# Optimization experiments

Hardware: AMD Instinct MI355X
Metric: run time of the kernel (lower is better)

Reference implementation:

```python
import jax, jax.numpy as jnp
import numpy as np

N = 100000      # nodes
E = 1600000     # edges (avg degree 16)
F_IN = 128      # num_node_features
H = 128         # hidden_size
C = 64          # num_classes


def sage_conv(x, src, dst, W_l, W_r, b, num_nodes):
    """PyG SAGEConv (mean aggr): out = lin_l(mean_{j->i} x_j) + lin_r(x_i) + b."""
    msg = x[src]                                                  # [E, F] gather
    agg = jax.ops.segment_sum(msg, dst, num_segments=num_nodes)   # [N, F] scatter-add
    deg = jax.ops.segment_sum(jnp.ones((src.shape[0],), x.dtype), dst,
                              num_segments=num_nodes)             # [N]
    agg = agg / jnp.maximum(deg, 1.0)[:, None]                    # mean (safe for isolated nodes)
    return agg @ W_l + x @ W_r + b


def setup_inputs() -> dict:
    key = jax.random.key(0)
    ks = jax.random.split(key, 8)
    x = jax.random.normal(ks[0], (N, F_IN), dtype=jnp.float32)
    edge_index = jax.random.randint(ks[1], (2, E), 0, N, dtype=jnp.int32).astype(jnp.int64)
    W1_l = jax.random.normal(ks[2], (F_IN, H), dtype=jnp.float32) / np.float32(np.sqrt(F_IN))
    W1_r = jax.random.normal(ks[3], (F_IN, H), dtype=jnp.float32) / np.float32(np.sqrt(F_IN))
    b1 = jnp.zeros((H,), jnp.float32)
    W2_l = jax.random.normal(ks[4], (H, C), dtype=jnp.float32) / np.float32(np.sqrt(H))
    W2_r = jax.random.normal(ks[5], (H, C), dtype=jnp.float32) / np.float32(np.sqrt(H))
    b2 = jnp.zeros((C,), jnp.float32)
    return {"x": x, "edge_index": edge_index,
            "W1_l": W1_l, "W1_r": W1_r, "b1": b1,
            "W2_l": W2_l, "W2_r": W2_r, "b2": b2}


def reference(x, edge_index, W1_l, W1_r, b1, W2_l, W2_r, b2):
    src, dst = edge_index[0], edge_index[1]
    h = jax.nn.relu(sage_conv(x, src, dst, W1_l, W1_r, b1, N))   # dropout: eval mode => identity
    logits = sage_conv(h, src, dst, W2_l, W2_r, b2, N)
    return jax.nn.log_softmax(logits, axis=1)
```

## Files before the change

### kernel.cpp

```cpp
#include <hip/hip_runtime.h>

#define Nn 100000
#define Ee 1600000
#define FIN 128
#define HID 128
#define CLS 64
#define NB 196
#define BCAP 9216

typedef unsigned short ushort_t;
typedef unsigned int uint_t;
typedef __attribute__((ext_vector_type(8))) short bf16x8;
typedef __attribute__((ext_vector_type(4))) float f32x4;

__device__ __forceinline__ ushort_t f2bf(float f) {
    uint_t u = __float_as_uint(f);
    return (ushort_t)((u + 0x7fffu + ((u >> 16) & 1u)) >> 16);
}
__device__ __forceinline__ float bflo(uint_t u) { return __uint_as_float(u << 16); }
__device__ __forceinline__ float bfhi(uint_t u) { return __uint_as_float(u & 0xffff0000u); }


__global__ __launch_bounds__(1024) void k_front(const int* __restrict__ src,
                                                const int* __restrict__ dst,
                                                int* __restrict__ bcur,
                                                uint2* __restrict__ bedge,
                                                const float* __restrict__ x,
                                                ushort_t* __restrict__ xb,
                                                const float* __restrict__ W1l,
                                                const float* __restrict__ W1r,
                                                const float* __restrict__ W2l,
                                                const float* __restrict__ W2r,
                                                ushort_t* __restrict__ w1lt,
                                                ushort_t* __restrict__ w1rt,
                                                ushort_t* __restrict__ w2lt,
                                                ushort_t* __restrict__ w2rt) {
    __shared__ int h[NB];
    __shared__ int lbase[NB];
    int b = blockIdx.x;
    int t = threadIdx.x;
    if (b < NB) {
        if (t < NB) h[t] = 0;
        __syncthreads();
        int base = b * 8192;
        int bk[8], loc[8];
        #pragma unroll
        for (int it = 0; it < 8; ++it) {
            int e = base + it * 1024 + t;
            if (e < Ee) {
                bk[it] = dst[e] >> 9;
                loc[it] = atomicAdd(&h[bk[it]], 1);
            }
        }
        __syncthreads();
        if (t < NB && h[t]) lbase[t] = atomicAdd(&bcur[t], h[t]);
        __syncthreads();
        #pragma unroll
        for (int it = 0; it < 8; ++it) {
            int e = base + it * 1024 + t;
            if (e < Ee) {
                int pos = lbase[bk[it]] + loc[it];
                if (pos < BCAP)
                    bedge[(size_t)bk[it] * BCAP + pos] = make_uint2((uint_t)src[e], (uint_t)dst[e]);
            }
        }
    } else if (b < NB + 3125) {
        int i = (b - NB) * 1024 + t;
        float4 v = reinterpret_cast<const float4*>(x)[i];
        ushort4 o;
        o.x = f2bf(v.x); o.y = f2bf(v.y); o.z = f2bf(v.z); o.w = f2bf(v.w);
        reinterpret_cast<ushort4*>(xb)[i] = o;
    } else {
        int j = b - (NB + 3125);
        const float* Wsrc; ushort_t* Wdst; int Ncols; int cb;
        if (j < 16)      { Wsrc = W1l; Wdst = w1lt; Ncols = 128; cb = j; }
        else if (j < 32) { Wsrc = W1r; Wdst = w1rt; Ncols = 128; cb = j - 16; }
        else if (j < 40) { Wsrc = W2l; Wdst = w2lt; Ncols = 64;  cb = j - 32; }
        else             { Wsrc = W2r; Wdst = w2rt; Ncols = 64;  cb = j - 40; }
        int i = cb * 1024 + t;
        if (i < 128 * Ncols) {
            int k = i / Ncols, n = i % Ncols;
            Wdst[(size_t)n * 128 + k] = f2bf(Wsrc[i]);
        }
    }
}

__global__ __launch_bounds__(256) void k_bscan(const int* __restrict__ bcur,
                                               int* __restrict__ bstart,
                                               int* __restrict__ rowptr) {
    __shared__ int s[256];
    int t = threadIdx.x;
    int v = (t < NB) ? min(bcur[t], BCAP) : 0;
    s[t] = v;
    __syncthreads();
    for (int off = 1; off < 256; off <<= 1) {
        int u = (t >= off) ? s[t - off] : 0;
        __syncthreads();
        s[t] += u;
        __syncthreads();
    }
    if (t < NB) bstart[t] = s[t] - v;
    if (t == NB - 1) { bstart[NB] = s[t]; rowptr[Nn] = s[t]; }
}

__global__ __launch_bounds__(1024) void k_fillB(const uint2* __restrict__ bedge,
                                                const int* __restrict__ bcur,
                                                const int* __restrict__ bstart,
                                                int* __restrict__ rowptr,
                                                int* __restrict__ csr) {
    __shared__ int h[512];
    __shared__ int off[512];
    int b = blockIdx.x, t = threadIdx.x;
    if (t < 512) h[t] = 0;
    __syncthreads();
    int n = min(bcur[b], BCAP);
    int node0 = b << 9;
    const uint2* be = bedge + (size_t)b * BCAP;
    for (int i = t; i < n; i += 1024)
        atomicAdd(&h[(int)be[i].y - node0], 1);
    __syncthreads();
    if (t < 512) off[t] = h[t];
    __syncthreads();
    for (int o = 1; o < 512; o <<= 1) {
        int v = (t < 512 && t >= o) ? off[t - o] : 0;
        __syncthreads();
        if (t < 512) off[t] += v;
        __syncthreads();
    }
    int base_ = bstart[b];
    if (t < 512) {
        int excl = off[t] - h[t];
        int node = node0 + t;
        if (node < Nn) rowptr[node] = base_ + excl;
        h[t] = excl;
    }
    __syncthreads();
    for (int i = t; i < n; i += 1024) {
        uint2 ed = be[i];
        int loc = atomicAdd(&h[(int)ed.y - node0], 1);
        csr[base_ + loc] = (int)ed.x;
    }
}


__global__ __launch_bounds__(256) void k_agg1(const ushort_t* __restrict__ xb,
                                              const int* __restrict__ rowptr,
                                              const int* __restrict__ csr,
                                              ushort_t* __restrict__ outb) {
    int wid = (blockIdx.x * blockDim.x + threadIdx.x) >> 6;
    int lane = threadIdx.x & 63;
    if (wid >= Nn) return;
    int s0 = __builtin_amdgcn_readfirstlane(rowptr[wid]);
    int s1 = __builtin_amdgcn_readfirstlane(rowptr[wid + 1]);
    float ax = 0.f, ay = 0.f;
    int e = s0;
    for (; e + 16 <= s1; e += 16) {
        int idx[16];
        #pragma unroll
        for (int j = 0; j < 16; ++j) idx[j] = __builtin_amdgcn_readfirstlane(csr[e + j]);
        uint_t u[16];
        #pragma unroll
        for (int j = 0; j < 16; ++j)
            u[j] = *reinterpret_cast<const uint_t*>(xb + (size_t)idx[j] * 128 + lane * 2);
        #pragma unroll
        for (int j = 0; j < 16; ++j) { ax += bflo(u[j]); ay += bfhi(u[j]); }
    }
    for (; e + 8 <= s1; e += 8) {
        int idx[8];
        #pragma unroll
        for (int j = 0; j < 8; ++j) idx[j] = __builtin_amdgcn_readfirstlane(csr[e + j]);
        uint_t u[8];
        #pragma unroll
        for (int j = 0; j < 8; ++j)
            u[j] = *reinterpret_cast<const uint_t*>(xb + (size_t)idx[j] * 128 + lane * 2);
        #pragma unroll
        for (int j = 0; j < 8; ++j) { ax += bflo(u[j]); ay += bfhi(u[j]); }
    }
    for (; e < s1; ++e) {
        int s = __builtin_amdgcn_readfirstlane(csr[e]);
        uint_t u = *reinterpret_cast<const uint_t*>(xb + (size_t)s * 128 + lane * 2);
        ax += bflo(u); ay += bfhi(u);
    }
    float invd = (s1 > s0) ? 1.0f / (float)(s1 - s0) : 0.0f;
    uint_t o = (uint_t)f2bf(ax * invd) | ((uint_t)f2bf(ay * invd) << 16);
    *reinterpret_cast<uint_t*>(outb + (size_t)wid * 128 + lane * 2) = o;
}


__global__ __launch_bounds__(512) void k_gemm1m(const ushort_t* __restrict__ Ab0,
                                                const ushort_t* __restrict__ Ab1,
                                                const ushort_t* __restrict__ Wt0,
                                                const ushort_t* __restrict__ Wt1,
                                                const float* __restrict__ bias,
                                                ushort_t* __restrict__ hb) {
    __shared__ ushort_t lw[2 * 16384];
    const int tid = threadIdx.x;
    char* lwc = reinterpret_cast<char*>(lw);
    #pragma unroll
    for (int i = 0; i < 8; ++i) {
        int c = tid + i * 512;
        int pair = c >> 11;
        int col = (c & 2047) >> 4;
        int kc = c & 15;
        const ushort_t* Wsrc = pair ? Wt1 : Wt0;
        uint4 v = *reinterpret_cast<const uint4*>(Wsrc + col * 128 + kc * 8);
        int dst = ((pair << 15) | (col << 8) | (kc << 4)) ^ ((col & 7) << 4);
        *reinterpret_cast<uint4*>(lwc + dst) = v;
    }
    __syncthreads();

    int gw = (blockIdx.x * 512 + tid) >> 6;
    int lane = tid & 63;
    if (gw >= Nn / 16) return;
    int row0 = gw * 16;
    int r = lane & 15;
    int kg = lane >> 4;
    f32x4 acc[8];
    #pragma unroll
    for (int c = 0; c < 8; ++c) acc[c] = (f32x4){0.f, 0.f, 0.f, 0.f};
    #pragma unroll
    for (int pair = 0; pair < 2; ++pair) {
        const ushort_t* A = pair ? Ab1 : Ab0;
        #pragma unroll
        for (int ks = 0; ks < 4; ++ks) {
            int kbase = ks * 32 + kg * 8;
            bf16x8 af = *reinterpret_cast<const bf16x8*>(A + (size_t)(row0 + r) * 128 + kbase);
            #pragma unroll
            for (int c = 0; c < 8; ++c) {
                int boff = ((pair << 15) | ((c * 16 + r) << 8) | (ks * 64 + kg * 16))
                           ^ ((r & 7) << 4);
                bf16x8 bf = *reinterpret_cast<const bf16x8*>(lwc + boff);
                acc[c] = __builtin_amdgcn_mfma_f32_16x16x32_bf16(af, bf, acc[c], 0, 0, 0);
            }
        }
    }
    #pragma unroll
    for (int c = 0; c < 8; ++c) {
        float bv = bias[c * 16 + r];
        #pragma unroll
        for (int i = 0; i < 4; ++i) {
            int row = row0 + kg * 4 + i;
            hb[(size_t)row * 128 + c * 16 + r] = f2bf(fmaxf(acc[c][i] + bv, 0.f));
        }
    }
}

__global__ __launch_bounds__(256) void k_gemm2f(const ushort_t* __restrict__ Ab,
                                                const ushort_t* __restrict__ Wtl,
                                                const ushort_t* __restrict__ Wtr,
                                                ushort_t* __restrict__ tb,
                                                float* __restrict__ outu) {
    int gw = (blockIdx.x * 256 + threadIdx.x) >> 6;
    int lane = threadIdx.x & 63;
    if (gw >= Nn / 16) return;
    int row0 = gw * 16;
    int r = lane & 15;
    int kg = lane >> 4;
    f32x4 accL[4], accR[4];
    #pragma unroll
    for (int c = 0; c < 4; ++c) {
        accL[c] = (f32x4){0.f, 0.f, 0.f, 0.f};
        accR[c] = (f32x4){0.f, 0.f, 0.f, 0.f};
    }
    #pragma unroll
    for (int ks = 0; ks < 4; ++ks) {
        int kbase = ks * 32 + kg * 8;
        bf16x8 af = *reinterpret_cast<const bf16x8*>(Ab + (size_t)(row0 + r) * 128 + kbase);
        #pragma unroll
        for (int c = 0; c < 4; ++c) {
            bf16x8 bl = *reinterpret_cast<const bf16x8*>(Wtl + (size_t)(c * 16 + r) * 128 + kbase);
            accL[c] = __builtin_amdgcn_mfma_f32_16x16x32_bf16(af, bl, accL[c], 0, 0, 0);
            bf16x8 br = *reinterpret_cast<const bf16x8*>(Wtr + (size_t)(c * 16 + r) * 128 + kbase);
            accR[c] = __builtin_amdgcn_mfma_f32_16x16x32_bf16(af, br, accR[c], 0, 0, 0);
        }
    }
    #pragma unroll
    for (int c = 0; c < 4; ++c) {
        #pragma unroll
        for (int i = 0; i < 4; ++i) {
            int row = row0 + kg * 4 + i;
            tb[(size_t)row * 64 + c * 16 + r] = f2bf(accL[c][i]);
            outu[(size_t)row * 64 + c * 16 + r] = accR[c][i];
        }
    }
}


__global__ __launch_bounds__(256) void k_logsm(float* __restrict__ out,
                                               const ushort_t* __restrict__ tb,
                                               const int* __restrict__ rowptr,
                                               const int* __restrict__ csr,
                                               const float* __restrict__ bias) {
    int wid = (blockIdx.x * blockDim.x + threadIdx.x) >> 6;
    int lane = threadIdx.x & 63;
    if (wid >= Nn) return;
    int s0 = __builtin_amdgcn_readfirstlane(rowptr[wid]);
    int s1 = __builtin_amdgcn_readfirstlane(rowptr[wid + 1]);
    float a = 0.f;
    int e = s0;
    for (; e + 16 <= s1; e += 16) {
        int idx[16];
        #pragma unroll
        for (int j = 0; j < 16; ++j) idx[j] = __builtin_amdgcn_readfirstlane(csr[e + j]);
        ushort_t u[16];
        #pragma unroll
        for (int j = 0; j < 16; ++j) u[j] = tb[(size_t)idx[j] * 64 + lane];
        #pragma unroll
        for (int j = 0; j < 16; ++j) a += __uint_as_float(((uint_t)u[j]) << 16);
    }
    for (; e + 8 <= s1; e += 8) {
        int idx[8];
        #pragma unroll
        for (int j = 0; j < 8; ++j) idx[j] = __builtin_amdgcn_readfirstlane(csr[e + j]);
        ushort_t u[8];
        #pragma unroll
        for (int j = 0; j < 8; ++j) u[j] = tb[(size_t)idx[j] * 64 + lane];
        #pragma unroll
        for (int j = 0; j < 8; ++j) a += __uint_as_float(((uint_t)u[j]) << 16);
    }
    for (; e < s1; ++e) {
        int s = __builtin_amdgcn_readfirstlane(csr[e]);
        a += __uint_as_float(((uint_t)tb[(size_t)s * 64 + lane]) << 16);
    }
    float invd = (s1 > s0) ? 1.0f / (float)(s1 - s0) : 0.0f;
    size_t o = (size_t)wid * 64 + lane;
    float v = (out[o] + a * invd) + bias[lane];
    float m = v;
    #pragma unroll
    for (int off = 32; off; off >>= 1) m = fmaxf(m, __shfl_xor(m, off));
    float ex = __expf(v - m);
    float s_ = ex;
    #pragma unroll
    for (int off = 32; off; off >>= 1) s_ += __shfl_xor(s_, off);
    out[o] = v - m - __logf(s_);
}


extern "C" void kernel_launch(void* const* d_in, const int* in_sizes, int n_in,
                              void* d_out, int out_size, void* d_ws, size_t ws_size,
                              hipStream_t stream) {
    const float* x   = (const float*)d_in[0];
    const int*   ei  = (const int*)d_in[1];
    const float* W1l = (const float*)d_in[2];
    const float* W1r = (const float*)d_in[3];
    const float* b1  = (const float*)d_in[4];
    const float* W2l = (const float*)d_in[5];
    const float* W2r = (const float*)d_in[6];
    const float* b2  = (const float*)d_in[7];
    float* out = (float*)d_out;

    char* ws = (char*)d_ws;
    int*      bstart = (int*)(ws + 0);
    int*      rowptr = (int*)(ws + 800768);
    int*      csr    = (int*)(ws + 1201152);
    ushort_t* xb     = (ushort_t*)(ws + 7601152);
    ushort_t* aggb   = (ushort_t*)(ws + 33201152);
    ushort_t* w1lt   = (ushort_t*)(ws + 58801152);
    ushort_t* w1rt   = (ushort_t*)(ws + 58833920);
    ushort_t* w2lt   = (ushort_t*)(ws + 58866688);
    ushort_t* w2rt   = (ushort_t*)(ws + 58883072);
    uint2*    bedge  = (uint2*)(ws + 60000000);
    int*      bcur   = (int*)(ws + 74450688);
    ushort_t* hb     = (ushort_t*)(ws + 84401152);
    ushort_t* tb     = (ushort_t*)(ws + 7601152);

    const int* src = ei;
    const int* dst = ei + Ee;

    hipMemsetAsync(bcur, 0, NB * 4, stream);

    k_front<<<NB + 3125 + 48, 1024, 0, stream>>>(src, dst, bcur, bedge, x, xb,
                                                 W1l, W1r, W2l, W2r,
                                                 w1lt, w1rt, w2lt, w2rt);
    k_bscan<<<1, 256, 0, stream>>>(bcur, bstart, rowptr);
    k_fillB<<<NB, 1024, 0, stream>>>(bedge, bcur, bstart, rowptr, csr);

    k_agg1<<<(Nn + 3) / 4, 256, 0, stream>>>(xb, rowptr, csr, aggb);
    k_gemm1m<<<(Nn / 16 + 7) / 8, 512, 0, stream>>>(aggb, xb, w1lt, w1rt, b1, hb);

    k_gemm2f<<<(Nn / 16 + 3) / 4, 256, 0, stream>>>(hb, w2lt, w2rt, tb, out);
    k_logsm<<<(Nn + 3) / 4, 256, 0, stream>>>(out, tb, rowptr, csr, b2);
}
```

Baseline: 210.2 us.

## Gather layer-1 neighbor features in FP8 and fold bucket scan into fillB

Adds an FP8 (e4m3) copy of x, written in the front kernel, and switches the layer-1 mean aggregation to gather 1 byte per feature instead of bf16, halving the random-gather traffic. It also removes the separate single-block bucket scan kernel: each fillB block recomputes the 196-entry prefix sum itself, saving one launch. The cost is an extra write of the FP8 copy and a large loss of precision in the aggregated features, since e4m3 has only 3 mantissa bits, which may exceed the accuracy tolerance.

```diff
diff --git a/kernel.cpp b/kernel.cpp
--- a/kernel.cpp
+++ b/kernel.cpp
@@ -9,9 +9,11 @@
 #define BCAP 9216
 
 typedef unsigned short ushort_t;
+typedef unsigned char uchar_t;
 typedef unsigned int uint_t;
 typedef __attribute__((ext_vector_type(8))) short bf16x8;
 typedef __attribute__((ext_vector_type(4))) float f32x4;
+typedef __attribute__((ext_vector_type(2))) float f32x2;
 
 __device__ __forceinline__ ushort_t f2bf(float f) {
     uint_t u = __float_as_uint(f);
@@ -27,6 +29,7 @@
                                                 uint2* __restrict__ bedge,
                                                 const float* __restrict__ x,
                                                 ushort_t* __restrict__ xb,
+                                                uint_t* __restrict__ xq,
                                                 const float* __restrict__ W1l,
                                                 const float* __restrict__ W1r,
                                                 const float* __restrict__ W2l,
@@ -70,6 +73,9 @@
         ushort4 o;
         o.x = f2bf(v.x); o.y = f2bf(v.y); o.z = f2bf(v.z); o.w = f2bf(v.w);
         reinterpret_cast<ushort4*>(xb)[i] = o;
+        int q = __builtin_amdgcn_cvt_pk_fp8_f32(v.x, v.y, 0, false);
+        q = __builtin_amdgcn_cvt_pk_fp8_f32(v.z, v.w, q, true);
+        xq[i] = (uint_t)q;
     } else {
         int j = b - (NB + 3125);
         const float* Wsrc; ushort_t* Wdst; int Ncols; int cb;
@@ -85,37 +91,31 @@
     }
 }
 
-__global__ __launch_bounds__(256) void k_bscan(const int* __restrict__ bcur,
-                                               int* __restrict__ bstart,
-                                               int* __restrict__ rowptr) {
-    __shared__ int s[256];
-    int t = threadIdx.x;
-    int v = (t < NB) ? min(bcur[t], BCAP) : 0;
-    s[t] = v;
-    __syncthreads();
-    for (int off = 1; off < 256; off <<= 1) {
-        int u = (t >= off) ? s[t - off] : 0;
-        __syncthreads();
-        s[t] += u;
-        __syncthreads();
-    }
-    if (t < NB) bstart[t] = s[t] - v;
-    if (t == NB - 1) { bstart[NB] = s[t]; rowptr[Nn] = s[t]; }
-}
-
 __global__ __launch_bounds__(1024) void k_fillB(const uint2* __restrict__ bedge,
                                                 const int* __restrict__ bcur,
-                                                const int* __restrict__ bstart,
                                                 int* __restrict__ rowptr,
                                                 int* __restrict__ csr) {
     __shared__ int h[512];
     __shared__ int off[512];
+    __shared__ int sbase;
     int b = blockIdx.x, t = threadIdx.x;
-    if (t < 512) h[t] = 0;
-    __syncthreads();
+    if (t < 256) off[t] = (t < NB) ? min(bcur[t], BCAP) : 0;
+    __syncthreads();
+    for (int o = 1; o < 256; o <<= 1) {
+        int v = (t < 256 && t >= o) ? off[t - o] : 0;
+        __syncthreads();
+        if (t < 256) off[t] += v;
+        __syncthreads();
+    }
+    if (t == 0) sbase = off[b] - min(bcur[b], BCAP);
+    if (b == NB - 1 && t == 0) rowptr[Nn] = off[NB - 1];
+    __syncthreads();
+    int base_ = sbase;
     int n = min(bcur[b], BCAP);
     int node0 = b << 9;
     const uint2* be = bedge + (size_t)b * BCAP;
+    if (t < 512) h[t] = 0;
+    __syncthreads();
     for (int i = t; i < n; i += 1024)
         atomicAdd(&h[(int)be[i].y - node0], 1);
     __syncthreads();
@@ -127,7 +127,6 @@
         if (t < 512) off[t] += v;
         __syncthreads();
     }
-    int base_ = bstart[b];
     if (t < 512) {
         int excl = off[t] - h[t];
         int node = node0 + t;
@@ -143,7 +142,7 @@
 }
 
 
-__global__ __launch_bounds__(256) void k_agg1(const ushort_t* __restrict__ xb,
+__global__ __launch_bounds__(256) void k_agg1(const uchar_t* __restrict__ xq,
                                               const int* __restrict__ rowptr,
                                               const int* __restrict__ csr,
                                               ushort_t* __restrict__ outb) {
@@ -158,28 +157,35 @@
         int idx[16];
         #pragma unroll
         for (int j = 0; j < 16; ++j) idx[j] = __builtin_amdgcn_readfirstlane(csr[e + j]);
-        uint_t u[16];
+        ushort_t u[16];
         #pragma unroll
         for (int j = 0; j < 16; ++j)
-            u[j] = *reinterpret_cast<const uint_t*>(xb + (size_t)idx[j] * 128 + lane * 2);
-        #pragma unroll
-        for (int j = 0; j < 16; ++j) { ax += bflo(u[j]); ay += bfhi(u[j]); }
+            u[j] = *reinterpret_cast<const ushort_t*>(xq + (size_t)idx[j] * 128 + lane * 2);
+        #pragma unroll
+        for (int j = 0; j < 16; ++j) {
+            f32x2 f = __builtin_amdgcn_cvt_pk_f32_fp8((int)u[j], false);
+            ax += f.x; ay += f.y;
+        }
     }
     for (; e + 8 <= s1; e += 8) {
         int idx[8];
         #pragma unroll
         for (int j = 0; j < 8; ++j) idx[j] = __builtin_amdgcn_readfirstlane(csr[e + j]);
-        uint_t u[8];
+        ushort_t u[8];
         #pragma unroll
         for (int j = 0; j < 8; ++j)
-            u[j] = *reinterpret_cast<const uint_t*>(xb + (size_t)idx[j] * 128 + lane * 2);
-        #pragma unroll
-        for (int j = 0; j < 8; ++j) { ax += bflo(u[j]); ay += bfhi(u[j]); }
+            u[j] = *reinterpret_cast<const ushort_t*>(xq + (size_t)idx[j] * 128 + lane * 2);
+        #pragma unroll
+        for (int j = 0; j < 8; ++j) {
+            f32x2 f = __builtin_amdgcn_cvt_pk_f32_fp8((int)u[j], false);
+            ax += f.x; ay += f.y;
+        }
     }
     for (; e < s1; ++e) {
         int s = __builtin_amdgcn_readfirstlane(csr[e]);
-        uint_t u = *reinterpret_cast<const uint_t*>(xb + (size_t)s * 128 + lane * 2);
-        ax += bflo(u); ay += bfhi(u);
+        ushort_t u = *reinterpret_cast<const ushort_t*>(xq + (size_t)s * 128 + lane * 2);
+        f32x2 f = __builtin_amdgcn_cvt_pk_f32_fp8((int)u, false);
+        ax += f.x; ay += f.y;
     }
     float invd = (s1 > s0) ? 1.0f / (float)(s1 - s0) : 0.0f;
     uint_t o = (uint_t)f2bf(ax * invd) | ((uint_t)f2bf(ay * invd) << 16);
@@ -350,7 +356,6 @@
     float* out = (float*)d_out;
 
     char* ws = (char*)d_ws;
-    int*      bstart = (int*)(ws + 0);
     int*      rowptr = (int*)(ws + 800768);
     int*      csr    = (int*)(ws + 1201152);
     ushort_t* xb     = (ushort_t*)(ws + 7601152);
@@ -361,6 +366,7 @@
     ushort_t* w2rt   = (ushort_t*)(ws + 58883072);
     uint2*    bedge  = (uint2*)(ws + 60000000);
     int*      bcur   = (int*)(ws + 74450688);
+    uint_t*   xq     = (uint_t*)(ws + 74451968);
     ushort_t* hb     = (ushort_t*)(ws + 84401152);
     ushort_t* tb     = (ushort_t*)(ws + 7601152);
 
@@ -369,13 +375,12 @@
 
     hipMemsetAsync(bcur, 0, NB * 4, stream);
 
-    k_front<<<NB + 3125 + 48, 1024, 0, stream>>>(src, dst, bcur, bedge, x, xb,
+    k_front<<<NB + 3125 + 48, 1024, 0, stream>>>(src, dst, bcur, bedge, x, xb, xq,
                                                  W1l, W1r, W2l, W2r,
                                                  w1lt, w1rt, w2lt, w2rt);
-    k_bscan<<<1, 256, 0, stream>>>(bcur, bstart, rowptr);
-    k_fillB<<<NB, 1024, 0, stream>>>(bedge, bcur, bstart, rowptr, csr);
-
-    k_agg1<<<(Nn + 3) / 4, 256, 0, stream>>>(xb, rowptr, csr, aggb);
+    k_fillB<<<NB, 1024, 0, stream>>>(bedge, bcur, rowptr, csr);
+
+    k_agg1<<<(Nn + 3) / 4, 256, 0, stream>>>((const uchar_t*)xq, rowptr, csr, aggb);
     k_gemm1m<<<(Nn / 16 + 7) / 8, 512, 0, stream>>>(aggb, xb, w1lt, w1rt, b1, hb);
 
     k_gemm2f<<<(Nn / 16 + 3) / 4, 256, 0, stream>>>(hb, w2lt, w2rt, tb, out);
```

After: 198.7 us. -5.5%, faster.
